# Kernel tuning notes

Measured on AMD Instinct MI355X. Metric: run time of the kernel, lower is better.

## Reference

```python
import jax, jax.numpy as jnp
import numpy as np

FILTER_SIZE = (9, 9)
N_ITER = 5  # training-mode iteration count (module forces 5 in train, 10 in eval)
DN = ('NCHW', 'OIHW', 'NCHW')


def _gauss_kernel1d(inv_theta, spacing, fsize):
    half = fsize // 2
    d = spacing * jnp.arange(-half, half + 1, dtype=jnp.float32)
    k = jnp.exp(-(d * inv_theta) ** 2 / 2)
    # zero out the center tap (message passing excludes self)
    return k * (jnp.arange(fsize) != half).astype(k.dtype)


def _blur_single(x, spacing, inv_theta):
    # x: (C, H, W); separable gaussian filtering with 'same' output via pre-padding
    ph, pw = FILTER_SIZE[0] // 2, FILTER_SIZE[1] // 2
    xp = jnp.pad(x, ((0, 0), (ph, ph), (pw, pw)))[:, None]  # (C, 1, H+2ph, W+2pw)
    kh = _gauss_kernel1d(inv_theta[0], spacing[0], FILTER_SIZE[0])
    kw = _gauss_kernel1d(inv_theta[1], spacing[1], FILTER_SIZE[1])
    xp = jax.lax.conv_general_dilated(xp, kh[None, None, :, None], (1, 1), 'VALID', dimension_numbers=DN)
    xp = jax.lax.conv_general_dilated(xp, kw[None, None, None, :], (1, 1), 'VALID', dimension_numbers=DN)
    return xp[:, 0]  # (C, H, W)


def setup_inputs() -> dict:
    key = jax.random.key(0)
    k1, _ = jax.random.split(key)
    B, H, W, C = 16, 384, 384, 21
    x = jax.random.normal(k1, (B, H, W, C), dtype=jnp.float32)
    spatial_spacings = jnp.ones((B, 2), dtype=jnp.float32)
    smoothness_weight = jnp.asarray(1.0, dtype=jnp.float32)
    inv_smoothness_theta = jnp.full((2,), 1.0 / 0.5, dtype=jnp.float32)  # 1/theta
    return {
        'x': x,
        'spatial_spacings': spatial_spacings,
        'smoothness_weight': smoothness_weight,
        'inv_smoothness_theta': inv_smoothness_theta,
    }


def reference(x, spatial_spacings, smoothness_weight, inv_smoothness_theta):
    xt = jnp.transpose(x, (0, 3, 1, 2))  # (B, C, H, W)
    negative_unary = xt
    C = xt.shape[1]
    # compatibility: -(l1 == l2) -> -I_C
    compat = -jnp.eye(C, dtype=xt.dtype)
    blur = jax.vmap(_blur_single, in_axes=(0, 0, None))

    def body(xc, _):
        p = jax.nn.softmax(xc, axis=1)
        s = smoothness_weight * blur(p, spatial_spacings, inv_smoothness_theta)
        c = jnp.einsum('bjhw,jk->bkhw', s, compat)
        return negative_unary - c, None

    xt, _ = jax.lax.scan(body, xt, None, length=N_ITER)
    # returns == 'logits'
    return jnp.transpose(xt, (0, 2, 3, 1))
```

## Files before the change

kernel.cpp:

```cpp
#include <hip/hip_runtime.h>
#include <hip/hip_fp16.h>


#define BB    16
#define Himg  384
#define Wimg  384
#define CC    21
#define NP    11
#define TH    16
#define TW    16
#define RR    4
#define PH    (TH + 2*RR)
#define PW    (TW + 2*RR)
#define NPIX  (PH * PW)
#define PLANE_B 2384
#define ROW_B   (PW * 4)
#define NTASK (PW * NP)

static __device__ __forceinline__ unsigned int pk_add(unsigned int a, unsigned int b) {
    unsigned int d; asm("v_pk_add_f16 %0, %1, %2" : "=v"(d) : "v"(a), "v"(b)); return d;
}
static __device__ __forceinline__ unsigned int pk_mul(unsigned int a, unsigned int b) {
    unsigned int d; asm("v_pk_mul_f16 %0, %1, %2" : "=v"(d) : "v"(a), "v"(b)); return d;
}
static __device__ __forceinline__ unsigned int pk_fma(unsigned int a, unsigned int b, unsigned int c) {
    unsigned int d; asm("v_pk_fma_f16 %0, %1, %2, %3" : "=v"(d) : "v"(a), "v"(b), "v"(c)); return d;
}

__global__ __launch_bounds__(256, 6)
void crf_iter_kernel(const float* __restrict__ xin,
                     const float* __restrict__ unary,
                     float* __restrict__ out,
                     const float* __restrict__ spacings,
                     const float* __restrict__ inv_theta,
                     const float* __restrict__ sw_ptr)
{
    __shared__ __align__(16) unsigned char smem[NP * PLANE_B];

    const int tid = threadIdx.x;
    const int b   = blockIdx.z;
    const int h0  = blockIdx.y * TH;
    const int w0  = blockIdx.x * TW;

    const float sp_h = spacings[b * 2 + 0];
    const float sp_w = spacings[b * 2 + 1];
    const float ith  = inv_theta[0];
    const float itw  = inv_theta[1];
    const float sw   = sw_ptr[0];
    unsigned int khp[4], kwp[4];
#pragma unroll
    for (int i = 0; i < 4; ++i) {
        float dh = sp_h * (float)(i - 4) * ith;
        float dw = sp_w * (float)(i - 4) * itw;
        float kh = __expf(-0.5f * dh * dh);
        float kw = sw * __expf(-0.5f * dw * dw);
        __half2 a = __floats2half2_rn(kh, kh);
        __half2 c = __floats2half2_rn(kw, kw);
        khp[i] = *(unsigned int*)&a;
        kwp[i] = *(unsigned int*)&c;
    }

    for (int p = tid; p < NPIX; p += 256) {
        const int r  = p / PW;
        const int px = p - r * PW;
        const int hh = h0 - RR + r;
        const int gw = w0 - RR + px;
        unsigned char* lbase = smem + p * 4;
        if (hh >= 0 && hh < Himg && gw >= 0 && gw < Wimg) {
            const float* gp = xin + ((b * Himg + hh) * Wimg + gw) * CC;
            float v[CC];
#pragma unroll
            for (int c = 0; c < CC; ++c) v[c] = gp[c];
            float m = v[0];
#pragma unroll
            for (int c = 1; c < CC; ++c) m = fmaxf(m, v[c]);
            float s = 0.f;
#pragma unroll
            for (int c = 0; c < CC; ++c) { v[c] = __expf(v[c] - m); s += v[c]; }
            const float inv = 1.0f / s;
#pragma unroll
            for (int cp = 0; cp < 10; ++cp) {
                __half2 hx = __floats2half2_rn(v[2*cp] * inv, v[2*cp+1] * inv);
                *(__half2*)(lbase + cp * PLANE_B) = hx;
            }
            __half2 hl = __floats2half2_rn(v[20] * inv, 0.f);
            *(__half2*)(lbase + 10 * PLANE_B) = hl;
        } else {
            const __half2 z = __floats2half2_rn(0.f, 0.f);
#pragma unroll
            for (int cp = 0; cp < NP; ++cp)
                *(__half2*)(lbase + cp * PLANE_B) = z;
        }
    }
    __syncthreads();

    for (int t = tid; t < NTASK; t += 256) {
        const int cp  = t / PW;
        const int col = t - cp * PW;
        unsigned char* base = smem + cp * PLANE_B + col * 4;
        unsigned int v[PH];
#pragma unroll
        for (int r = 0; r < PH; ++r) v[r] = *(const unsigned int*)(base + r * ROW_B);
#pragma unroll
        for (int tt = 0; tt < TH; ++tt) {
            unsigned int s0 = pk_add(v[tt],     v[tt + 8]);
            unsigned int s1 = pk_add(v[tt + 1], v[tt + 7]);
            unsigned int s2 = pk_add(v[tt + 2], v[tt + 6]);
            unsigned int s3 = pk_add(v[tt + 3], v[tt + 5]);
            unsigned int acc = pk_mul(khp[0], s0);
            acc = pk_fma(khp[1], s1, acc);
            acc = pk_fma(khp[2], s2, acc);
            acc = pk_fma(khp[3], s3, acc);
            *(unsigned int*)(base + tt * ROW_B) = acc;
        }
    }
    __syncthreads();

    if (tid < TH * NP) {
        const int h  = tid / NP;
        const int cp = tid - h * NP;
        unsigned char* base = smem + cp * PLANE_B + h * ROW_B;
        unsigned int v[PW];
#pragma unroll
        for (int k = 0; k < 6; ++k) {
            const uint4 q = *(const uint4*)(base + k * 16);
            v[4*k+0] = q.x; v[4*k+1] = q.y; v[4*k+2] = q.z; v[4*k+3] = q.w;
        }
        unsigned int o[TW];
#pragma unroll
        for (int wt = 0; wt < TW; ++wt) {
            unsigned int s0 = pk_add(v[wt],     v[wt + 8]);
            unsigned int s1 = pk_add(v[wt + 1], v[wt + 7]);
            unsigned int s2 = pk_add(v[wt + 2], v[wt + 6]);
            unsigned int s3 = pk_add(v[wt + 3], v[wt + 5]);
            unsigned int acc = pk_mul(kwp[0], s0);
            acc = pk_fma(kwp[1], s1, acc);
            acc = pk_fma(kwp[2], s2, acc);
            acc = pk_fma(kwp[3], s3, acc);
            o[wt] = acc;
        }
#pragma unroll
        for (int k = 0; k < 4; ++k) {
            uint4 wq;
            wq.x = o[4*k+0]; wq.y = o[4*k+1]; wq.z = o[4*k+2]; wq.w = o[4*k+3];
            *(uint4*)(base + k * 16) = wq;
        }
    }
    __syncthreads();

    {
        const int r  = tid >> 4;
        const int px = tid & 15;
        unsigned char* lbase = smem + (r * PW + px) * 4;
        float sv[CC + 1];
#pragma unroll
        for (int cp = 0; cp < NP; ++cp) {
            float2 f = __half22float2(*(const __half2*)(lbase + cp * PLANE_B));
            sv[2*cp] = f.x; sv[2*cp+1] = f.y;
        }
        const int g = ((b * Himg + h0 + r) * Wimg + (w0 + px)) * CC;
        const float* up = unary + g;
        float* op = out + g;
#pragma unroll
        for (int c = 0; c < CC; ++c) op[c] = up[c] + sv[c];
    }
}

extern "C" void kernel_launch(void* const* d_in, const int* in_sizes, int n_in,
                              void* d_out, int out_size, void* d_ws, size_t ws_size,
                              hipStream_t stream) {
    const float* x         = (const float*)d_in[0];
    const float* spacings  = (const float*)d_in[1];
    const float* sw        = (const float*)d_in[2];
    const float* inv_theta = (const float*)d_in[3];
    float* out = (float*)d_out;
    float* ws  = (float*)d_ws;

    dim3 grid(Wimg / TW, Himg / TH, BB);
    dim3 block(256);

    crf_iter_kernel<<<grid, block, 0, stream>>>(x,   x, out, spacings, inv_theta, sw);
    crf_iter_kernel<<<grid, block, 0, stream>>>(out, x, ws,  spacings, inv_theta, sw);
    crf_iter_kernel<<<grid, block, 0, stream>>>(ws,  x, out, spacings, inv_theta, sw);
    crf_iter_kernel<<<grid, block, 0, stream>>>(out, x, ws,  spacings, inv_theta, sw);
    crf_iter_kernel<<<grid, block, 0, stream>>>(ws,  x, out, spacings, inv_theta, sw);
}
```

Baseline: 918.9 us.

## Coalesce global loads/stores via channel-contiguous staging and vectorized epilogue

The halo tile is now loaded with consecutive threads reading consecutive floats of each image row and staged as fp16 in shared memory, and softmax runs from shared memory afterwards. Previously each thread read 21 strided floats per pixel. The unary tile is prefetched into registers as float4 before the softmax, and the final add-and-store is written as coalesced float4 chunks. This costs an extra barrier, clamped-address loads for out-of-range columns, more registers, and a round of input rounding to fp16 before the softmax, which may shift precision.

```diff
diff --git a/kernel.cpp b/kernel.cpp
--- a/kernel.cpp
+++ b/kernel.cpp
@@ -13,9 +13,13 @@
 #define PH    (TH + 2*RR)
 #define PW    (TW + 2*RR)
 #define NPIX  (PH * PW)
+#define ROWF_F (PW * CC)
 #define PLANE_B 2384
 #define ROW_B   (PW * 4)
 #define NTASK (PW * NP)
+#define NTOT  (BB * Himg * Wimg * CC)
+#define RCHUNKS (TW * CC / 4)
+#define NCHUNK5 (TH * RCHUNKS)
 
 static __device__ __forceinline__ unsigned int pk_add(unsigned int a, unsigned int b) {
     unsigned int d; asm("v_pk_add_f16 %0, %1, %2" : "=v"(d) : "v"(a), "v"(b)); return d;
@@ -60,6 +64,35 @@
         kwp[i] = *(unsigned int*)&c;
     }
 
+    for (int qq = tid; qq < ROWF_F; qq += 256) {
+        const int px = qq / CC;
+        const int c  = qq - px * CC;
+        unsigned char* dst = smem + (c >> 1) * PLANE_B + px * 4 + ((c & 1) << 1);
+        int basef = ((b * Himg + (h0 - RR)) * Wimg + (w0 - RR)) * CC + qq;
+#pragma unroll
+        for (int r = 0; r < PH; ++r) {
+            const int hh = h0 - RR + r;
+            if (hh >= 0 && hh < Himg) {
+                int a = basef < 0 ? 0 : (basef > NTOT - 1 ? NTOT - 1 : basef);
+                *(__half*)(dst + r * ROW_B) = __float2half_rn(xin[a]);
+            }
+            basef += Wimg * CC;
+        }
+    }
+
+    const int gbase = ((b * Himg + h0) * Wimg + w0) * CC;
+    float4 uf[6];
+#pragma unroll
+    for (int k = 0; k < 6; ++k) {
+        const int j = tid + k * 256;
+        if (j < NCHUNK5) {
+            const int hrow = j / RCHUNKS;
+            const int qq   = j - hrow * RCHUNKS;
+            uf[k] = *(const float4*)(unary + gbase + hrow * (Wimg * CC) + qq * 4);
+        }
+    }
+    __syncthreads();
+
     for (int p = tid; p < NPIX; p += 256) {
         const int r  = p / PW;
         const int px = p - r * PW;
@@ -67,10 +100,12 @@
         const int gw = w0 - RR + px;
         unsigned char* lbase = smem + p * 4;
         if (hh >= 0 && hh < Himg && gw >= 0 && gw < Wimg) {
-            const float* gp = xin + ((b * Himg + hh) * Wimg + gw) * CC;
-            float v[CC];
-#pragma unroll
-            for (int c = 0; c < CC; ++c) v[c] = gp[c];
+            float v[22];
+#pragma unroll
+            for (int cp = 0; cp < NP; ++cp) {
+                float2 f = __half22float2(*(const __half2*)(lbase + cp * PLANE_B));
+                v[2*cp] = f.x; v[2*cp+1] = f.y;
+            }
             float m = v[0];
 #pragma unroll
             for (int c = 1; c < CC; ++c) m = fmaxf(m, v[c]);
@@ -79,12 +114,10 @@
             for (int c = 0; c < CC; ++c) { v[c] = __expf(v[c] - m); s += v[c]; }
             const float inv = 1.0f / s;
 #pragma unroll
-            for (int cp = 0; cp < 10; ++cp) {
-                __half2 hx = __floats2half2_rn(v[2*cp] * inv, v[2*cp+1] * inv);
-                *(__half2*)(lbase + cp * PLANE_B) = hx;
-            }
-            __half2 hl = __floats2half2_rn(v[20] * inv, 0.f);
-            *(__half2*)(lbase + 10 * PLANE_B) = hl;
+            for (int cp = 0; cp < 10; ++cp)
+                *(__half2*)(lbase + cp * PLANE_B) =
+                    __floats2half2_rn(v[2*cp] * inv, v[2*cp+1] * inv);
+            *(__half2*)(lbase + 10 * PLANE_B) = __floats2half2_rn(v[20] * inv, 0.f);
         } else {
             const __half2 z = __floats2half2_rn(0.f, 0.f);
 #pragma unroll
@@ -148,21 +181,31 @@
     }
     __syncthreads();
 
-    {
-        const int r  = tid >> 4;
-        const int px = tid & 15;
-        unsigned char* lbase = smem + (r * PW + px) * 4;
-        float sv[CC + 1];
-#pragma unroll
-        for (int cp = 0; cp < NP; ++cp) {
-            float2 f = __half22float2(*(const __half2*)(lbase + cp * PLANE_B));
-            sv[2*cp] = f.x; sv[2*cp+1] = f.y;
-        }
-        const int g = ((b * Himg + h0 + r) * Wimg + (w0 + px)) * CC;
-        const float* up = unary + g;
-        float* op = out + g;
-#pragma unroll
-        for (int c = 0; c < CC; ++c) op[c] = up[c] + sv[c];
+#pragma unroll
+    for (int k = 0; k < 6; ++k) {
+        const int j = tid + k * 256;
+        if (j < NCHUNK5) {
+            const int hrow = j / RCHUNKS;
+            const int qq   = j - hrow * RCHUNKS;
+            const int f    = qq * 4;
+            int px = f / 21;
+            int c  = f - px * 21;
+            int addr = (c >> 1) * PLANE_B + hrow * ROW_B + px * 4 + (c & 1) * 2;
+            float sv[4];
+#pragma unroll
+            for (int i = 0; i < 4; ++i) {
+                sv[i] = __half2float(*(const __half*)(smem + addr));
+                const int wrap = (c == 20);
+                const int odd  = c & 1;
+                addr += wrap ? (4 - 10 * PLANE_B) : (odd ? (PLANE_B - 2) : 2);
+                c = wrap ? 0 : c + 1;
+            }
+            const float4 u = uf[k];
+            float4 o;
+            o.x = u.x + sv[0]; o.y = u.y + sv[1];
+            o.z = u.z + sv[2]; o.w = u.w + sv[3];
+            *(float4*)(out + gbase + hrow * (Wimg * CC) + qq * 4) = o;
+        }
     }
 }
 
```

New measurement: 1.269 ms. 1.38x slower.

## Vectorize output epilogue with float4 row chunks and swizzle tile order

Applied to the files above, without the earlier changes.

The final unary-add and store phase now walks each tile row as contiguous float4 chunks of the channel-interleaved output. It gathers the four matching half values from the shared-memory channel planes with incremental address stepping, instead of having each thread write 21 scalar floats for a single pixel. The block index is also remapped so consecutively launched blocks fall on tiles spread across the image, which aims to balance memory-channel or cache usage. The trade-off is more scalar index arithmetic and scattered 2-byte LDS reads in exchange for coalesced 16-byte global accesses.

```diff
diff --git a/kernel.cpp b/kernel.cpp
--- a/kernel.cpp
+++ b/kernel.cpp
@@ -16,6 +16,9 @@
 #define PLANE_B 2384
 #define ROW_B   (PW * 4)
 #define NTASK (PW * NP)
+#define RCHUNKS (TW * CC / 4)
+#define NCHUNK5 (TH * RCHUNKS)
+#define NTILES  (24 * 24 * BB)
 
 static __device__ __forceinline__ unsigned int pk_add(unsigned int a, unsigned int b) {
     unsigned int d; asm("v_pk_add_f16 %0, %1, %2" : "=v"(d) : "v"(a), "v"(b)); return d;
@@ -38,9 +41,14 @@
     __shared__ __align__(16) unsigned char smem[NP * PLANE_B];
 
     const int tid = threadIdx.x;
-    const int b   = blockIdx.z;
-    const int h0  = blockIdx.y * TH;
-    const int w0  = blockIdx.x * TW;
+
+    const int lin = blockIdx.x + 24 * (blockIdx.y + 24 * blockIdx.z);
+    const int swz = (lin & 7) * (NTILES / 8) + (lin >> 3);
+    const int b   = swz / 576;
+    const int rem = swz - b * 576;
+    const int ty  = rem / 24;
+    const int h0  = ty * TH;
+    const int w0  = (rem - ty * 24) * TW;
 
     const float sp_h = spacings[b * 2 + 0];
     const float sp_w = spacings[b * 2 + 1];
@@ -149,20 +157,30 @@
     __syncthreads();
 
     {
-        const int r  = tid >> 4;
-        const int px = tid & 15;
-        unsigned char* lbase = smem + (r * PW + px) * 4;
-        float sv[CC + 1];
-#pragma unroll
-        for (int cp = 0; cp < NP; ++cp) {
-            float2 f = __half22float2(*(const __half2*)(lbase + cp * PLANE_B));
-            sv[2*cp] = f.x; sv[2*cp+1] = f.y;
-        }
-        const int g = ((b * Himg + h0 + r) * Wimg + (w0 + px)) * CC;
-        const float* up = unary + g;
-        float* op = out + g;
-#pragma unroll
-        for (int c = 0; c < CC; ++c) op[c] = up[c] + sv[c];
+        const int gbase = ((b * Himg + h0) * Wimg + w0) * CC;
+        for (int j = tid; j < NCHUNK5; j += 256) {
+            const int hrow = j / RCHUNKS;
+            const int qq   = j - hrow * RCHUNKS;
+            const int f    = qq * 4;
+            int px = f / 21;
+            int c  = f - px * 21;
+            int addr = (c >> 1) * PLANE_B + hrow * ROW_B + px * 4 + (c & 1) * 2;
+            float sv[4];
+#pragma unroll
+            for (int i = 0; i < 4; ++i) {
+                sv[i] = __half2float(*(const __half*)(smem + addr));
+                const int wrap = (c == 20);
+                const int odd  = c & 1;
+                addr += wrap ? (4 - 10 * PLANE_B) : (odd ? (PLANE_B - 2) : 2);
+                c = wrap ? 0 : c + 1;
+            }
+            const int g = gbase + hrow * (Wimg * CC) + f;
+            const float4 u = *(const float4*)(unary + g);
+            float4 o;
+            o.x = u.x + sv[0]; o.y = u.y + sv[1];
+            o.z = u.z + sv[2]; o.w = u.w + sv[3];
+            *(float4*)(out + g) = o;
+        }
     }
 }
 
```

Measured after the change: 820.3 us. 1.12x faster.
